# Performance work log

Hardware: AMD Instinct MI355X
Metric: run time of the kernel (lower is better)

## Reference

```python
import jax, jax.numpy as jnp
import numpy as np

GAMMA_BASE = 0.0   # self.gamma for pt >= 0.5
GAMMA_MID = 3.0    # 0.2 <= pt < 0.5
GAMMA_LOW = 5.0    # pt < 0.2


def setup_inputs() -> dict:
    key = jax.random.key(0)
    k1, k2 = jax.random.split(key)
    N, C = 32768, 4096
    inp = jax.random.normal(k1, (N, C), dtype=jnp.float32)
    target = jax.random.randint(k2, (N,), 0, C, dtype=jnp.int32)
    return {"input": inp, "target": target}


def reference(input, target):
    # log_softmax over classes, gather log-prob of the true class: [N]
    logpt = jax.nn.log_softmax(input, axis=1)
    logpt = jnp.take_along_axis(logpt, target[:, None].astype(jnp.int32), axis=1)[:, 0]
    pt = jnp.exp(logpt)
    # vectorized replacement of the per-sample Python loop in get_gamma_list
    gamma = jnp.where(pt >= 0.5, GAMMA_BASE,
                      jnp.where(pt < 0.2, GAMMA_LOW, GAMMA_MID))
    loss = -((1.0 - pt) ** gamma) * logpt
    return loss.sum()  # size_average=False
```

## Files before the change

kernel.cpp:

```cpp
#include <hip/hip_runtime.h>


#define CCONST 4096
#define ROW_THREADS 256
#define ROWS_PER_BLOCK 4

__global__ __launch_bounds__(ROW_THREADS) void focal_row_kernel(
    const float* __restrict__ inp,
    const int* __restrict__ target,
    float* __restrict__ partial,
    int n_rows)
{
    const int lane = threadIdx.x & 63;
    const int wave = threadIdx.x >> 6;
    const int row  = blockIdx.x * ROWS_PER_BLOCK + wave;
    if (row >= n_rows) return;

    const float4* rowp = reinterpret_cast<const float4*>(inp + (size_t)row * CCONST);

    float4 v[16];
#pragma unroll
    for (int k = 0; k < 16; ++k)
        v[k] = rowp[lane + 64 * k];

    const int c  = target[row];
    const float xt = inp[(size_t)row * CCONST + c];

    float m = -INFINITY;
#pragma unroll
    for (int k = 0; k < 16; ++k)
        m = fmaxf(m, fmaxf(fmaxf(v[k].x, v[k].y), fmaxf(v[k].z, v[k].w)));
#pragma unroll
    for (int off = 32; off > 0; off >>= 1)
        m = fmaxf(m, __shfl_xor(m, off));

    float s = 0.0f;
#pragma unroll
    for (int k = 0; k < 16; ++k) {
        s += __expf(v[k].x - m) + __expf(v[k].y - m)
           + __expf(v[k].z - m) + __expf(v[k].w - m);
    }
#pragma unroll
    for (int off = 32; off > 0; off >>= 1)
        s += __shfl_xor(s, off);

    if (lane == 0) {
        float logpt = xt - m - __logf(s);
        float pt = __expf(logpt);
        float u = 1.0f - pt;
        float w;
        if (pt >= 0.5f) {
            w = 1.0f;
        } else if (pt < 0.2f) {
            float u2 = u * u;
            w = u2 * u2 * u;
        } else {
            w = u * u * u;
        }
        partial[row] = -w * logpt;
    }
}

#define RED_THREADS 1024
__global__ __launch_bounds__(RED_THREADS) void focal_reduce_kernel(
    const float* __restrict__ partial,
    float* __restrict__ out,
    int n)
{
    const int t = threadIdx.x;
    float s = 0.0f;
#pragma unroll 4
    for (int i = t; i < n; i += RED_THREADS)
        s += partial[i];

#pragma unroll
    for (int off = 32; off > 0; off >>= 1)
        s += __shfl_xor(s, off);

    __shared__ float ssum[RED_THREADS / 64];
    if ((t & 63) == 0) ssum[t >> 6] = s;
    __syncthreads();
    if (t == 0) {
        float tot = 0.0f;
#pragma unroll
        for (int i = 0; i < RED_THREADS / 64; ++i)
            tot += ssum[i];
        out[0] = tot;
    }
}

extern "C" void kernel_launch(void* const* d_in, const int* in_sizes, int n_in,
                              void* d_out, int out_size, void* d_ws, size_t ws_size,
                              hipStream_t stream)
{
    const float* inp    = (const float*)d_in[0];
    const int*   target = (const int*)d_in[1];
    float* out = (float*)d_out;
    float* partial = (float*)d_ws;

    const int N = in_sizes[1];

    const int blocks = (N + ROWS_PER_BLOCK - 1) / ROWS_PER_BLOCK;
    focal_row_kernel<<<blocks, ROW_THREADS, 0, stream>>>(inp, target, partial, N);
    focal_reduce_kernel<<<1, RED_THREADS, 0, stream>>>(partial, out, N);
}
```

Baseline: 102.7 us.

## Use persistent waves looping over row chunks with per-block loss accumulation

The row kernel moves from one wave per row over 8192 blocks to a fixed grid of 1024 blocks, with each wave handling a contiguous chunk of 8 rows. Each wave accumulates its loss in a register and each block writes one partial. The final reduction reads only 1024 values. The softmax exponentials are rewritten as exp2f of an FMA with log2(e), and launch bounds now hint 4 blocks per CU. The goal is less block scheduling overhead, a smaller reduction, and cheaper exp arithmetic. The cost is fewer waves in flight for a memory-bound stream and no overlap of loads across rows inside a wave.

Result: slower. 105.8 us (+3.0%).

```diff
diff --git a/kernel.cpp b/kernel.cpp
--- a/kernel.cpp
+++ b/kernel.cpp
@@ -2,10 +2,14 @@
 
 
 #define CCONST 4096
-#define ROW_THREADS 256
-#define ROWS_PER_BLOCK 4
+#define THREADS 256
+#define WAVES_PER_BLOCK 4
+#define BLOCKS 1024
+#define TOTAL_WAVES (BLOCKS * WAVES_PER_BLOCK)
 
-__global__ __launch_bounds__(ROW_THREADS) void focal_row_kernel(
+#define LOG2E 1.44269504088896340736f
+
+__global__ __launch_bounds__(THREADS, 4) void focal_row_kernel(
     const float* __restrict__ inp,
     const int* __restrict__ target,
     float* __restrict__ partial,
@@ -13,38 +17,45 @@
 {
     const int lane = threadIdx.x & 63;
     const int wave = threadIdx.x >> 6;
-    const int row  = blockIdx.x * ROWS_PER_BLOCK + wave;
-    if (row >= n_rows) return;
+    const int wave_global = blockIdx.x * WAVES_PER_BLOCK + wave;
 
-    const float4* rowp = reinterpret_cast<const float4*>(inp + (size_t)row * CCONST);
+    const int rows_per_wave = (n_rows + TOTAL_WAVES - 1) / TOTAL_WAVES;
+    const int row0 = wave_global * rows_per_wave;
 
-    float4 v[16];
+    float loss_acc = 0.0f;
+
+    for (int r = 0; r < rows_per_wave; ++r) {
+        const int row = row0 + r;
+        if (row >= n_rows) break;
+
+        const int c = target[row];
+        const float xt = inp[(size_t)row * CCONST + c];
+
+        const float4* rowp = reinterpret_cast<const float4*>(inp + (size_t)row * CCONST);
+        float4 v[16];
 #pragma unroll
-    for (int k = 0; k < 16; ++k)
-        v[k] = rowp[lane + 64 * k];
+        for (int k = 0; k < 16; ++k)
+            v[k] = rowp[lane + 64 * k];
 
-    const int c  = target[row];
-    const float xt = inp[(size_t)row * CCONST + c];
+        float m = -INFINITY;
+#pragma unroll
+        for (int k = 0; k < 16; ++k)
+            m = fmaxf(m, fmaxf(fmaxf(v[k].x, v[k].y), fmaxf(v[k].z, v[k].w)));
+#pragma unroll
+        for (int off = 32; off > 0; off >>= 1)
+            m = fmaxf(m, __shfl_xor(m, off));
 
-    float m = -INFINITY;
+        const float mk = -m * LOG2E;
+        float s = 0.0f;
 #pragma unroll
-    for (int k = 0; k < 16; ++k)
-        m = fmaxf(m, fmaxf(fmaxf(v[k].x, v[k].y), fmaxf(v[k].z, v[k].w)));
+        for (int k = 0; k < 16; ++k) {
+            s += exp2f(fmaf(v[k].x, LOG2E, mk)) + exp2f(fmaf(v[k].y, LOG2E, mk))
+               + exp2f(fmaf(v[k].z, LOG2E, mk)) + exp2f(fmaf(v[k].w, LOG2E, mk));
+        }
 #pragma unroll
-    for (int off = 32; off > 0; off >>= 1)
-        m = fmaxf(m, __shfl_xor(m, off));
+        for (int off = 32; off > 0; off >>= 1)
+            s += __shfl_xor(s, off);
 
-    float s = 0.0f;
-#pragma unroll
-    for (int k = 0; k < 16; ++k) {
-        s += __expf(v[k].x - m) + __expf(v[k].y - m)
-           + __expf(v[k].z - m) + __expf(v[k].w - m);
-    }
-#pragma unroll
-    for (int off = 32; off > 0; off >>= 1)
-        s += __shfl_xor(s, off);
-
-    if (lane == 0) {
         float logpt = xt - m - __logf(s);
         float pt = __expf(logpt);
         float u = 1.0f - pt;
@@ -57,36 +68,35 @@
         } else {
             w = u * u * u;
         }
-        partial[row] = -w * logpt;
+        loss_acc += -w * logpt;
     }
+
+    __shared__ float ls[WAVES_PER_BLOCK];
+    if (lane == 0) ls[wave] = loss_acc;
+    __syncthreads();
+    if (threadIdx.x == 0)
+        partial[blockIdx.x] = (ls[0] + ls[1]) + (ls[2] + ls[3]);
 }
 
-#define RED_THREADS 1024
-__global__ __launch_bounds__(RED_THREADS) void focal_reduce_kernel(
+__global__ __launch_bounds__(THREADS) void focal_reduce_kernel(
     const float* __restrict__ partial,
-    float* __restrict__ out,
-    int n)
+    float* __restrict__ out)
 {
     const int t = threadIdx.x;
     float s = 0.0f;
-#pragma unroll 4
-    for (int i = t; i < n; i += RED_THREADS)
-        s += partial[i];
+#pragma unroll
+    for (int i = 0; i < BLOCKS / THREADS; ++i)
+        s += partial[t + THREADS * i];
 
 #pragma unroll
     for (int off = 32; off > 0; off >>= 1)
         s += __shfl_xor(s, off);
 
-    __shared__ float ssum[RED_THREADS / 64];
+    __shared__ float ssum[THREADS / 64];
     if ((t & 63) == 0) ssum[t >> 6] = s;
     __syncthreads();
-    if (t == 0) {
-        float tot = 0.0f;
-#pragma unroll
-        for (int i = 0; i < RED_THREADS / 64; ++i)
-            tot += ssum[i];
-        out[0] = tot;
-    }
+    if (t == 0)
+        out[0] = (ssum[0] + ssum[1]) + (ssum[2] + ssum[3]);
 }
 
 extern "C" void kernel_launch(void* const* d_in, const int* in_sizes, int n_in,
@@ -100,7 +110,6 @@
 
     const int N = in_sizes[1];
 
-    const int blocks = (N + ROWS_PER_BLOCK - 1) / ROWS_PER_BLOCK;
-    focal_row_kernel<<<blocks, ROW_THREADS, 0, stream>>>(inp, target, partial, N);
-    focal_reduce_kernel<<<1, RED_THREADS, 0, stream>>>(partial, out, N);
+    focal_row_kernel<<<BLOCKS, THREADS, 0, stream>>>(inp, target, partial, N);
+    focal_reduce_kernel<<<1, THREADS, 0, stream>>>(partial, out);
 }
```

## Split each row across two waves with LDS combine and nontemporal loads

Applied to the files above, without the earlier changes.

Each row is now handled by two wavefronts, each holding half the row (8 float4 per lane instead of 16). The two halves combine their max and sum through shared memory with block barriers. Loads use nontemporal hints, exp is computed as exp2 with a folded fma, and each block writes one partial sum so the final reduce reads half as many values. The aim is lower register pressure and more waves in flight to hide HBM latency on a bandwidth-bound pass, at the cost of extra barriers per block.

After: 85.67 us. 1.2x faster.

```diff
diff --git a/kernel.cpp b/kernel.cpp
--- a/kernel.cpp
+++ b/kernel.cpp
@@ -2,49 +2,69 @@
 
 
 #define CCONST 4096
-#define ROW_THREADS 256
-#define ROWS_PER_BLOCK 4
+#define THREADS 256
+#define ROWS_PER_BLOCK 2
+#define LOG2E 1.44269504088896340736f
 
-__global__ __launch_bounds__(ROW_THREADS) void focal_row_kernel(
+typedef float f32x4 __attribute__((ext_vector_type(4)));
+
+__global__ __launch_bounds__(THREADS) void focal_row_kernel(
     const float* __restrict__ inp,
     const int* __restrict__ target,
     float* __restrict__ partial,
     int n_rows)
 {
-    const int lane = threadIdx.x & 63;
-    const int wave = threadIdx.x >> 6;
-    const int row  = blockIdx.x * ROWS_PER_BLOCK + wave;
-    if (row >= n_rows) return;
+    const int t     = threadIdx.x;
+    const int lane  = t & 63;
+    const int wave  = t >> 6;
+    const int rhalf = wave & 1;
+    const int rloc  = wave >> 1;
+    const int row   = blockIdx.x * ROWS_PER_BLOCK + rloc;
 
-    const float4* rowp = reinterpret_cast<const float4*>(inp + (size_t)row * CCONST);
+    __shared__ float sm[4];
+    __shared__ float ss[4];
+    __shared__ float lsum[ROWS_PER_BLOCK];
 
-    float4 v[16];
+    float loss = 0.0f;
+    if (row < n_rows) {
+        const float* rowbase = inp + (size_t)row * CCONST;
+
+        const int c = target[row];
+        const float xt = rowbase[c];
+
+        const f32x4* rowp = reinterpret_cast<const f32x4*>(rowbase) + rhalf * 512;
+        f32x4 v[8];
 #pragma unroll
-    for (int k = 0; k < 16; ++k)
-        v[k] = rowp[lane + 64 * k];
+        for (int k = 0; k < 8; ++k)
+            v[k] = __builtin_nontemporal_load(&rowp[lane + 64 * k]);
 
-    const int c  = target[row];
-    const float xt = inp[(size_t)row * CCONST + c];
+        float m = -INFINITY;
+#pragma unroll
+        for (int k = 0; k < 8; ++k)
+            m = fmaxf(m, fmaxf(fmaxf(v[k].x, v[k].y), fmaxf(v[k].z, v[k].w)));
+#pragma unroll
+        for (int off = 32; off > 0; off >>= 1)
+            m = fmaxf(m, __shfl_xor(m, off));
 
-    float m = -INFINITY;
+        if (lane == 0) sm[wave] = m;
+        __syncthreads();
+        m = fmaxf(sm[rloc * 2], sm[rloc * 2 + 1]);
+
+        const float mk = -m * LOG2E;
+        float s = 0.0f;
 #pragma unroll
-    for (int k = 0; k < 16; ++k)
-        m = fmaxf(m, fmaxf(fmaxf(v[k].x, v[k].y), fmaxf(v[k].z, v[k].w)));
+        for (int k = 0; k < 8; ++k) {
+            s += exp2f(fmaf(v[k].x, LOG2E, mk)) + exp2f(fmaf(v[k].y, LOG2E, mk))
+               + exp2f(fmaf(v[k].z, LOG2E, mk)) + exp2f(fmaf(v[k].w, LOG2E, mk));
+        }
 #pragma unroll
-    for (int off = 32; off > 0; off >>= 1)
-        m = fmaxf(m, __shfl_xor(m, off));
+        for (int off = 32; off > 0; off >>= 1)
+            s += __shfl_xor(s, off);
 
-    float s = 0.0f;
-#pragma unroll
-    for (int k = 0; k < 16; ++k) {
-        s += __expf(v[k].x - m) + __expf(v[k].y - m)
-           + __expf(v[k].z - m) + __expf(v[k].w - m);
-    }
-#pragma unroll
-    for (int off = 32; off > 0; off >>= 1)
-        s += __shfl_xor(s, off);
+        if (lane == 0) ss[wave] = s;
+        __syncthreads();
+        s = ss[rloc * 2] + ss[rloc * 2 + 1];
 
-    if (lane == 0) {
         float logpt = xt - m - __logf(s);
         float pt = __expf(logpt);
         float u = 1.0f - pt;
@@ -57,8 +77,16 @@
         } else {
             w = u * u * u;
         }
-        partial[row] = -w * logpt;
+        loss = -w * logpt;
+    } else {
+        __syncthreads();
+        __syncthreads();
     }
+
+    if ((wave & 1) == 0 && lane == 0) lsum[rloc] = loss;
+    __syncthreads();
+    if (t == 0)
+        partial[blockIdx.x] = lsum[0] + lsum[1];
 }
 
 #define RED_THREADS 1024
@@ -99,8 +127,8 @@
     float* partial = (float*)d_ws;
 
     const int N = in_sizes[1];
+    const int blocks = (N + ROWS_PER_BLOCK - 1) / ROWS_PER_BLOCK;
 
-    const int blocks = (N + ROWS_PER_BLOCK - 1) / ROWS_PER_BLOCK;
-    focal_row_kernel<<<blocks, ROW_THREADS, 0, stream>>>(inp, target, partial, N);
-    focal_reduce_kernel<<<1, RED_THREADS, 0, stream>>>(partial, out, N);
+    focal_row_kernel<<<blocks, THREADS, 0, stream>>>(inp, target, partial, N);
+    focal_reduce_kernel<<<1, RED_THREADS, 0, stream>>>(partial, out, blocks);
 }
```
